# Kernel tuning notes

Measured on AMD Instinct MI355X. Metric: run time of the kernel, lower is better.

## Reference

```python
import jax, jax.numpy as jnp
import numpy as np
import math

D_MODEL = 1024
NUM_HEADS = 16
D_K = D_MODEL // NUM_HEADS


def setup_inputs() -> dict:
    key = jax.random.key(0)
    ks = jax.random.split(key, 7)
    B, S = 2, 2048
    scale = 1.0 / math.sqrt(D_MODEL)
    inp = {
        "q": jax.random.normal(ks[0], (B, S, D_MODEL), dtype=jnp.float32),
        "k": jax.random.normal(ks[1], (B, S, D_MODEL), dtype=jnp.float32),
        "v": jax.random.normal(ks[2], (B, S, D_MODEL), dtype=jnp.float32),
        # Source module reuses q_linear for q, k, and v projections, so only
        # Wq/bq are needed for the input projections; out projection separate.
        "Wq": jax.random.normal(ks[3], (D_MODEL, D_MODEL), dtype=jnp.float32) * scale,
        "bq": jnp.zeros((D_MODEL,), dtype=jnp.float32),
        "Wo": jax.random.normal(ks[4], (D_MODEL, D_MODEL), dtype=jnp.float32) * scale,
        "bo": jnp.zeros((D_MODEL,), dtype=jnp.float32),
    }
    return inp


def _attention(q, k, v, Wq, bq, Wo, bo):
    B, S, _ = q.shape

    def proj(x):
        # [B,S,D] -> [B,H,S,d_k]
        y = jnp.einsum("bsd,de->bse", x, Wq) + bq
        return y.reshape(B, S, NUM_HEADS, D_K).transpose(0, 2, 1, 3)

    qh, kh, vh = proj(q), proj(k), proj(v)
    # scores: [B,H,S,S]
    scores = jnp.einsum("bhsd,bhtd->bhst", qh, kh) / math.sqrt(D_K)
    attn = jax.nn.softmax(scores, axis=-1)
    # dropout: eval-mode identity
    out = jnp.einsum("bhst,bhtd->bhsd", attn, vh)  # [B,H,S,d_k]
    out = out.transpose(0, 2, 1, 3).reshape(B, S, D_MODEL)
    return jnp.einsum("bsd,de->bse", out, Wo) + bo


def reference(q, k, v, Wq, bq, Wo, bo):
    return _attention(q, k, v, Wq, bq, Wo, bo)
```

## Files before the change

kernel.cpp:

```cpp
#include <hip/hip_runtime.h>
#include <hip/hip_bf16.h>

typedef unsigned short u16;
typedef unsigned int   u32;
typedef __attribute__((ext_vector_type(8))) short bf16x8;
typedef __attribute__((ext_vector_type(4))) float f32x4;
typedef __attribute__((ext_vector_type(16))) float f32x16;

#define SEQ     2048
#define DM      1024
#define NH      16
#define DKH     64
#define PER_SRC 4194304

__device__ __forceinline__ u16 f2bf(float f) {
    union { float f; u32 u; } c; c.f = f;
    return (u16)((c.u + 0x7fffu + ((c.u >> 16) & 1u)) >> 16);
}

__device__ __forceinline__ u32 cvt_pk_bf16(float lo, float hi) {
    u32 r;
    asm("v_cvt_pk_bf16_f32 %0, %1, %2" : "=v"(r) : "v"(lo), "v"(hi));
    return r;
}

__device__ __forceinline__ void gload_lds16(const void* g, void* l) {
    __builtin_amdgcn_global_load_lds((__attribute__((address_space(1))) void*)g,
                                     (__attribute__((address_space(3))) void*)l,
                                     16, 0, 0);
}

__global__ void cast_qkv(const float* __restrict__ q, const float* __restrict__ k,
                         const float* __restrict__ v, u16* __restrict__ xb) {
    const float* src = (blockIdx.y == 0) ? q : (blockIdx.y == 1) ? k : v;
    u16* dst = xb + (size_t)blockIdx.y * PER_SRC;
    size_t i = ((size_t)blockIdx.x * 256 + threadIdx.x) * 8;
    float4 a = *(const float4*)(src + i);
    float4 b = *(const float4*)(src + i + 4);
    bf16x8 o;
    o[0] = (short)f2bf(a.x); o[1] = (short)f2bf(a.y);
    o[2] = (short)f2bf(a.z); o[3] = (short)f2bf(a.w);
    o[4] = (short)f2bf(b.x); o[5] = (short)f2bf(b.y);
    o[6] = (short)f2bf(b.z); o[7] = (short)f2bf(b.w);
    *(bf16x8*)(dst + i) = o;
}

__global__ void wtrans(const float* __restrict__ Wq, const float* __restrict__ Wo,
                       u16* __restrict__ Wqt, u16* __restrict__ Wot) {
    const float* W = blockIdx.y ? Wo : Wq;
    u16* Wt       = blockIdx.y ? Wot : Wqt;
    int k0 = (blockIdx.x & 15) * 64;
    int n0 = (blockIdx.x >> 4) * 64;
    __shared__ __align__(16) float t[64][68];
    int tid = threadIdx.x;
    int r = tid >> 2, cs = (tid & 3) * 16;
    #pragma unroll
    for (int j = 0; j < 4; ++j) {
        float4 vv = *(const float4*)(W + (size_t)(k0 + r) * DM + n0 + cs + j * 4);
        *(float4*)&t[r][cs + j * 4] = vv;
    }
    __syncthreads();
    bf16x8 o0, o1;
    #pragma unroll
    for (int j = 0; j < 8; ++j) o0[j] = (short)f2bf(t[cs + j][r]);
    #pragma unroll
    for (int j = 0; j < 8; ++j) o1[j] = (short)f2bf(t[cs + 8 + j][r]);
    u16* dst = Wt + (size_t)(n0 + r) * DM + k0 + cs;
    *(bf16x8*)(dst)     = o0;
    *(bf16x8*)(dst + 8) = o1;
}

__global__ void vtrans(const u16* __restrict__ vh, u16* __restrict__ vt) {
    int bh = blockIdx.y, st = blockIdx.x;
    __shared__ u16 t[64][72];
    int tid = threadIdx.x;
    int r = tid >> 2, cs = (tid & 3) * 16;
    const u16* src = vh + ((size_t)bh * SEQ + st * 64 + r) * DKH + cs;
    bf16x8 v0 = *(const bf16x8*)(src);
    bf16x8 v1 = *(const bf16x8*)(src + 8);
    #pragma unroll
    for (int j = 0; j < 8; ++j) { t[r][cs + j] = (u16)v0[j]; t[r][cs + 8 + j] = (u16)v1[j]; }
    __syncthreads();
    bf16x8 o0, o1;
    #pragma unroll
    for (int j = 0; j < 8; ++j) o0[j] = (short)t[cs + j][r];
    #pragma unroll
    for (int j = 0; j < 8; ++j) o1[j] = (short)t[cs + 8 + j][r];
    u16* dst = vt + ((size_t)bh * DKH + r) * SEQ + st * 64 + cs;
    *(bf16x8*)(dst)     = o0;
    *(bf16x8*)(dst + 8) = o1;
}

template<int MODE>
__global__ __launch_bounds__(256)
void gemm_bt(const u16* __restrict__ Abase, const u16* __restrict__ Bt,
             const float* __restrict__ bias, void* __restrict__ outbase)
{
    __shared__ __align__(16) u16 Alds[128 * 64];
    __shared__ __align__(16) u16 Blds[128 * 64];

    const int tid  = threadIdx.x;
    const int wave = tid >> 6;
    const int lane = tid & 63;
    const int low4 = lane & 15;
    const int quad = lane >> 4;
    const int m0 = (blockIdx.x >> 3) * 128;
    const int n0 = (blockIdx.x & 7) * 128;
    const int wm = (wave >> 1) * 64, wn = (wave & 1) * 64;

    const u16* A = Abase + (size_t)blockIdx.z * PER_SRC;

    f32x4 acc[4][4] = {};

    for (int kt = 0; kt < DM / 64; ++kt) {
        #pragma unroll
        for (int it = 0; it < 4; ++it) {
            int seg  = it * 256 + tid;
            int row  = seg >> 3;
            int slot = seg & 7;
            int ss   = slot ^ (row & 7);
            const u16* srcA;
            if (MODE == 0) {
                srcA = A + (size_t)(m0 + row) * DM + kt * 64 + ss * 8;
            } else {
                int m = m0 + row;
                srcA = A + (((size_t)((m >> 11) * NH + kt)) * SEQ + (m & (SEQ - 1))) * DKH + ss * 8;
            }
            gload_lds16(srcA, &Alds[(it * 256 + wave * 64) * 8]);
            gload_lds16(Bt + (size_t)(n0 + row) * DM + kt * 64 + ss * 8,
                        &Blds[(it * 256 + wave * 64) * 8]);
        }
        __syncthreads();
        #pragma unroll
        for (int kk = 0; kk < 2; ++kk) {
            bf16x8 af[4], bfr[4];
            #pragma unroll
            for (int mi = 0; mi < 4; ++mi) {
                int row = wm + mi * 16 + low4;
                af[mi] = *(const bf16x8*)&Alds[row * 64 + (((kk * 4 + quad) ^ (row & 7)) * 8)];
            }
            #pragma unroll
            for (int ni = 0; ni < 4; ++ni) {
                int row = wn + ni * 16 + low4;
                bfr[ni] = *(const bf16x8*)&Blds[row * 64 + (((kk * 4 + quad) ^ (row & 7)) * 8)];
            }
            #pragma unroll
            for (int mi = 0; mi < 4; ++mi)
                #pragma unroll
                for (int ni = 0; ni < 4; ++ni)
                    acc[mi][ni] = __builtin_amdgcn_mfma_f32_16x16x32_bf16(
                        af[mi], bfr[ni], acc[mi][ni], 0, 0, 0);
        }
        __syncthreads();
    }

    #pragma unroll
    for (int mi = 0; mi < 4; ++mi) {
        #pragma unroll
        for (int ni = 0; ni < 4; ++ni) {
            int n = n0 + wn + ni * 16 + low4;
            float bv = bias[n];
            #pragma unroll
            for (int j = 0; j < 4; ++j) {
                int m = m0 + wm + mi * 16 + quad * 4 + j;
                float val = acc[mi][ni][j] + bv;
                if (MODE == 0) {
                    u16* dst = (u16*)outbase + (size_t)blockIdx.z * PER_SRC;
                    int b = m >> 11, s = m & (SEQ - 1);
                    int h = n >> 6, dd = n & 63;
                    dst[(size_t)(b * NH + h) * (SEQ * DKH) + (size_t)s * DKH + dd] = f2bf(val);
                } else {
                    ((float*)outbase)[(size_t)m * DM + n] = val;
                }
            }
        }
    }
}

__global__ __launch_bounds__(256, 2)
void attn(const u16* __restrict__ qh, const u16* __restrict__ kh,
          const u16* __restrict__ vt, u16* __restrict__ aoh)
{
    __shared__ __align__(16) u16 lds[2][8192];

    const int tid  = threadIdx.x;
    const int w    = tid >> 6;
    const int lane = tid & 63;
    const int l31  = lane & 31;
    const int hi   = lane >> 5;

    int bid = blockIdx.x;
    int lid = (bid & 7) * 64 + (bid >> 3);
    const int qt = lid & 15;
    const int bh = lid >> 4;

    const int qbase = qt * 128 + w * 32;
    const int q_row = qbase + l31;

    bf16x8 qf[4];
    #pragma unroll
    for (int c = 0; c < 4; ++c)
        qf[c] = *(const bf16x8*)&qh[((size_t)bh * SEQ + q_row) * DKH + c * 16 + hi * 8];

    float m_r = -1e30f, l_r = 0.f;
    f32x16 ot[2] = {};

#define STAGE(buf, kt_)                                                                 \
    {                                                                                   \
        _Pragma("unroll")                                                               \
        for (int it = 0; it < 2; ++it) {                                                \
            int seg  = it * 256 + tid;                                                  \
            int row  = seg >> 3;                                                        \
            int slot = seg & 7;                                                         \
            int ss   = slot ^ (row & 7);                                                \
            gload_lds16(kh + ((size_t)bh * SEQ + (kt_) * 64 + row) * DKH + ss * 8,      \
                        &lds[buf][(it * 256 + w * 64) * 8]);                            \
            gload_lds16(vt + ((size_t)bh * DKH + row) * SEQ + (kt_) * 64 + ss * 8,      \
                        &lds[buf][4096 + (it * 256 + w * 64) * 8]);                     \
        }                                                                               \
    }

    STAGE(0, 0);
    __syncthreads();

    int cur = 0;
    for (int kt = 0; kt < SEQ / 64; ++kt) {
        if (kt + 1 < SEQ / 64) STAGE(cur ^ 1, kt + 1);

        const u16* Klds = &lds[cur][0];
        const u16* Vlds = &lds[cur][4096];

        f32x16 st[2];
        #pragma unroll
        for (int T = 0; T < 2; ++T) {
            f32x16 acc = {};
            #pragma unroll
            for (int c = 0; c < 4; ++c) {
                int row = T * 32 + l31;
                bf16x8 kf = *(const bf16x8*)&Klds[row * 64 + (((c * 2 + hi) ^ (row & 7)) * 8)];
                acc = __builtin_amdgcn_mfma_f32_32x32x16_bf16(kf, qf[c], acc, 0, 0, 0);
            }
            st[T] = acc;
        }

        float mx[16];
        #pragma unroll
        for (int r = 0; r < 16; ++r) mx[r] = fmaxf(st[0][r], st[1][r]);
        #pragma unroll
        for (int s = 8; s > 0; s >>= 1)
            #pragma unroll
            for (int r = 0; r < 8; ++r) if (r < s) mx[r] = fmaxf(mx[r], mx[r + s]);
        float mloc = fmaxf(mx[0], __shfl_xor(mx[0], 32));
        float mnew = fmaxf(m_r, mloc * 0.125f);
        float fac  = __expf(m_r - mnew);
        m_r = mnew;
        float rs = 0.f;
        #pragma unroll
        for (int T = 0; T < 2; ++T)
            #pragma unroll
            for (int r = 0; r < 16; ++r) {
                float p = __expf(fmaf(st[T][r], 0.125f, -mnew));
                st[T][r] = p;
                rs += p;
            }
        rs += __shfl_xor(rs, 32);
        l_r = l_r * fac + rs;
        #pragma unroll
        for (int dt = 0; dt < 2; ++dt)
            #pragma unroll
            for (int r = 0; r < 16; ++r) ot[dt][r] *= fac;

        u32 pk[2][8];
        #pragma unroll
        for (int T = 0; T < 2; ++T)
            #pragma unroll
            for (int g = 0; g < 8; ++g)
                pk[T][g] = cvt_pk_bf16(st[T][2 * g], st[T][2 * g + 1]);

        bf16x8 pfrag[4];
        #pragma unroll
        for (int c = 0; c < 4; ++c) {
            int T = c >> 1, g0 = (c & 1) * 4;
            u32 wA = pk[T][g0], wB = pk[T][g0 + 1], wC = pk[T][g0 + 2], wD = pk[T][g0 + 3];
            u32 x0 = __shfl_xor(hi ? wA : wC, 32);
            u32 x1 = __shfl_xor(hi ? wB : wD, 32);
            union { bf16x8 v; u32 u[4]; } f;
            f.u[0] = hi ? x0 : wA;
            f.u[1] = hi ? x1 : wB;
            f.u[2] = hi ? wC : x0;
            f.u[3] = hi ? wD : x1;
            pfrag[c] = f.v;
        }

        #pragma unroll
        for (int dt = 0; dt < 2; ++dt)
            #pragma unroll
            for (int c = 0; c < 4; ++c) {
                int row = dt * 32 + l31;
                bf16x8 vf = *(const bf16x8*)&Vlds[row * 64 + (((c * 2 + hi) ^ (row & 7)) * 8)];
                ot[dt] = __builtin_amdgcn_mfma_f32_32x32x16_bf16(vf, pfrag[c], ot[dt], 0, 0, 0);
            }

        __syncthreads();
        cur ^= 1;
    }

    float inv = 1.0f / l_r;
    u16* tile = &lds[0][0] + w * 2048;
    #pragma unroll
    for (int dt = 0; dt < 2; ++dt)
        #pragma unroll
        for (int g = 0; g < 4; ++g) {
            u32 w0 = cvt_pk_bf16(ot[dt][4 * g] * inv,     ot[dt][4 * g + 1] * inv);
            u32 w1 = cvt_pk_bf16(ot[dt][4 * g + 2] * inv, ot[dt][4 * g + 3] * inv);
            int d0 = 8 * g + 4 * hi + 32 * dt;
            int byteoff = l31 * 128 + ((d0 * 2) ^ ((l31 & 7) << 4));
            uint2 pr; pr.x = w0; pr.y = w1;
            *(uint2*)((char*)tile + byteoff) = pr;
        }
    const size_t gbase = ((size_t)bh * SEQ + qbase) * DKH;
    #pragma unroll
    for (int p = 0; p < 4; ++p) {
        int q = p * 8 + (lane >> 3);
        int byteoff = q * 128 + (((lane & 7) * 16) ^ ((q & 7) << 4));
        bf16x8 val = *(const bf16x8*)((const char*)tile + byteoff);
        *(bf16x8*)&aoh[gbase + p * 512 + lane * 8] = val;
    }
#undef STAGE
}

extern "C" void kernel_launch(void* const* d_in, const int* in_sizes, int n_in,
                              void* d_out, int out_size, void* d_ws, size_t ws_size,
                              hipStream_t stream)
{
    const float* q  = (const float*)d_in[0];
    const float* k  = (const float*)d_in[1];
    const float* v  = (const float*)d_in[2];
    const float* Wq = (const float*)d_in[3];
    const float* bq = (const float*)d_in[4];
    const float* Wo = (const float*)d_in[5];
    const float* bo = (const float*)d_in[6];

    char* ws = (char*)d_ws;
    u16* xb  = (u16*)(ws);
    u16* wqt = (u16*)(ws + 25165824);
    u16* wot = (u16*)(ws + 27262976);
    u16* qh  = (u16*)(ws + 29360128);
    u16* kh  = qh + PER_SRC;
    u16* vh  = kh + PER_SRC;
    u16* vt  = (u16*)(ws);
    u16* aoh = (u16*)(ws + 8388608);

    cast_qkv<<<dim3(2048, 3), dim3(256), 0, stream>>>(q, k, v, xb);
    wtrans<<<dim3(256, 2), dim3(256), 0, stream>>>(Wq, Wo, wqt, wot);
    gemm_bt<0><<<dim3(256, 1, 3), dim3(256), 0, stream>>>(xb, wqt, bq, (void*)qh);
    vtrans<<<dim3(32, 32), dim3(256), 0, stream>>>(vh, vt);
    attn<<<dim3(512), dim3(256), 0, stream>>>(qh, kh, vt, aoh);
    gemm_bt<1><<<dim3(256), dim3(256), 0, stream>>>(aoh, wot, bo, d_out);
}
```

Baseline: 151.4 us.

## Use exp2 softmax with lazy rescale, tree max reduction, and MFMA priority hints

The online softmax now works in base 2 with a folded scale constant (log2(e)/8) and the raw exp2 intrinsic instead of __expf. The running-max rescale of the output accumulators is skipped unless some lane's new max exceeds the old one by more than a threshold. The max and sum reductions use shallower trees with several partial accumulators to shorten dependency chains. s_setprio raises wave priority around the MFMA blocks. The intent is to cut VALU work in the softmax, where the kernel spends much of its non-matrix time. The lazy rescale lets unnormalised values grow up to about 2^11.5, which costs a little bf16 precision headroom.

```diff
diff --git a/kernel.cpp b/kernel.cpp
--- a/kernel.cpp
+++ b/kernel.cpp
@@ -197,6 +197,8 @@
     const int qbase = qt * 128 + w * 32;
     const int q_row = qbase + l31;
 
+    const float SC = 0.18033688f;
+
     bf16x8 qf[4];
     #pragma unroll
     for (int c = 0; c < 4; ++c)
@@ -234,41 +236,54 @@
         #pragma unroll
         for (int T = 0; T < 2; ++T) {
             f32x16 acc = {};
+            __builtin_amdgcn_s_setprio(1);
             #pragma unroll
             for (int c = 0; c < 4; ++c) {
                 int row = T * 32 + l31;
                 bf16x8 kf = *(const bf16x8*)&Klds[row * 64 + (((c * 2 + hi) ^ (row & 7)) * 8)];
                 acc = __builtin_amdgcn_mfma_f32_32x32x16_bf16(kf, qf[c], acc, 0, 0, 0);
             }
+            __builtin_amdgcn_s_setprio(0);
             st[T] = acc;
         }
 
-        float mx[16];
-        #pragma unroll
-        for (int r = 0; r < 16; ++r) mx[r] = fmaxf(st[0][r], st[1][r]);
-        #pragma unroll
-        for (int s = 8; s > 0; s >>= 1)
-            #pragma unroll
-            for (int r = 0; r < 8; ++r) if (r < s) mx[r] = fmaxf(mx[r], mx[r + s]);
-        float mloc = fmaxf(mx[0], __shfl_xor(mx[0], 32));
-        float mnew = fmaxf(m_r, mloc * 0.125f);
-        float fac  = __expf(m_r - mnew);
-        m_r = mnew;
-        float rs = 0.f;
+        float mx[8];
+        #pragma unroll
+        for (int r = 0; r < 8; ++r)
+            mx[r] = fmaxf(fmaxf(st[0][r], st[0][r + 8]),
+                          fmaxf(st[1][r], st[1][r + 8]));
+        float t0 = fmaxf(fmaxf(mx[0], mx[1]), mx[2]);
+        float t1 = fmaxf(fmaxf(mx[3], mx[4]), mx[5]);
+        float t2 = fmaxf(mx[6], mx[7]);
+        float lmax = fmaxf(fmaxf(t0, t1), t2);
+        float mloc = fmaxf(lmax, __shfl_xor(lmax, 32)) * SC;
+
+        float mnew = fmaxf(m_r, mloc);
+        if (!__all(mloc <= m_r + 11.5f)) {
+            float fac = __builtin_amdgcn_exp2f(m_r - mnew);
+            m_r = mnew;
+            l_r *= fac;
+            #pragma unroll
+            for (int dt = 0; dt < 2; ++dt)
+                #pragma unroll
+                for (int r = 0; r < 16; ++r) ot[dt][r] *= fac;
+        }
+
+        float nm = -m_r;
+        float rs0 = 0.f, rs1 = 0.f, rs2 = 0.f, rs3 = 0.f;
         #pragma unroll
         for (int T = 0; T < 2; ++T)
             #pragma unroll
-            for (int r = 0; r < 16; ++r) {
-                float p = __expf(fmaf(st[T][r], 0.125f, -mnew));
-                st[T][r] = p;
-                rs += p;
-            }
-        rs += __shfl_xor(rs, 32);
-        l_r = l_r * fac + rs;
-        #pragma unroll
-        for (int dt = 0; dt < 2; ++dt)
-            #pragma unroll
-            for (int r = 0; r < 16; ++r) ot[dt][r] *= fac;
+            for (int r = 0; r < 16; r += 4) {
+                float p0 = __builtin_amdgcn_exp2f(fmaf(st[T][r],     SC, nm));
+                float p1 = __builtin_amdgcn_exp2f(fmaf(st[T][r + 1], SC, nm));
+                float p2 = __builtin_amdgcn_exp2f(fmaf(st[T][r + 2], SC, nm));
+                float p3 = __builtin_amdgcn_exp2f(fmaf(st[T][r + 3], SC, nm));
+                st[T][r] = p0; st[T][r + 1] = p1; st[T][r + 2] = p2; st[T][r + 3] = p3;
+                rs0 += p0; rs1 += p1; rs2 += p2; rs3 += p3;
+            }
+        float rsum = (rs0 + rs1) + (rs2 + rs3);
+        l_r += rsum + __shfl_xor(rsum, 32);
 
         u32 pk[2][8];
         #pragma unroll
@@ -292,6 +307,7 @@
             pfrag[c] = f.v;
         }
 
+        __builtin_amdgcn_s_setprio(1);
         #pragma unroll
         for (int dt = 0; dt < 2; ++dt)
             #pragma unroll
@@ -300,6 +316,7 @@
                 bf16x8 vf = *(const bf16x8*)&Vlds[row * 64 + (((c * 2 + hi) ^ (row & 7)) * 8)];
                 ot[dt] = __builtin_amdgcn_mfma_f32_32x32x16_bf16(vf, pfrag[c], ot[dt], 0, 0, 0);
             }
+        __builtin_amdgcn_s_setprio(0);
 
         __syncthreads();
         cur ^= 1;
```

After: 146.1 us. 1.04x faster.
